# Kernel optimization log

Measured on AMD Instinct MI355X. Metric: run time of the kernel, lower is better.

## Reference

```python
import jax, jax.numpy as jnp
import numpy as np
from jax import lax

B_, N, C, NH, KB = 4096, 64, 192, 6, 8
WH = WW = 8  # win_size
HD = C // NH
KS = 5  # depthwise kernel size (distance=2)


def _rel_pos_index(wh, ww, k_bound):
    ch = np.arange(wh); cw = np.arange(ww)
    coords = np.stack(np.meshgrid(ch, cw, indexing='ij'))  # (2, wh, ww)
    cf = coords.reshape(2, -1)
    rel = cf[:, :, None] - cf[:, None, :]
    rel = np.clip(rel, -(k_bound - 1), k_bound - 1).transpose(1, 2, 0).astype(np.int32)
    rel[..., 0] += k_bound - 1
    rel[..., 1] += k_bound - 1
    rel[..., 0] *= 2 * k_bound - 1
    return rel.sum(-1)  # (N, N) indices into (2k-1)^2 table


def setup_inputs() -> dict:
    key = jax.random.key(0)
    ks = jax.random.split(key, 12)
    s = 0.02
    x = jax.random.normal(ks[0], (B_, N, C), dtype=jnp.float32)
    wq = jax.random.normal(ks[1], (C, C), dtype=jnp.float32) * s
    bq = jnp.zeros((C,), dtype=jnp.float32)
    wkv = jax.random.normal(ks[2], (C, 3 * C), dtype=jnp.float32) * s
    bkv = jnp.zeros((3 * C,), dtype=jnp.float32)
    rpb_table = jax.random.normal(ks[3], ((2 * KB - 1) * (2 * KB - 1), NH), dtype=jnp.float32) * s
    rel_index = jnp.asarray(_rel_pos_index(WH, WW, KB), dtype=jnp.int32)
    dw_w = jax.random.normal(ks[4], (C, 1, KS, KS), dtype=jnp.float32) * s   # depthwise, groups=C
    dw_b = jnp.zeros((C,), dtype=jnp.float32)
    pw_w = jax.random.normal(ks[5], (C, C // NH, 1, 1), dtype=jnp.float32) * s  # 1x1, groups=NH
    pw_b = jnp.zeros((C,), dtype=jnp.float32)
    proj_w = jax.random.normal(ks[6], (C, C), dtype=jnp.float32) * s
    proj_b = jnp.zeros((C,), dtype=jnp.float32)
    return dict(x=x, wq=wq, bq=bq, wkv=wkv, bkv=bkv, rpb_table=rpb_table,
                rel_index=rel_index, dw_w=dw_w, dw_b=dw_b, pw_w=pw_w, pw_b=pw_b,
                proj_w=proj_w, proj_b=proj_b)


def reference(x, wq, bq, wkv, bkv, rpb_table, rel_index, dw_w, dw_b, pw_w, pw_b, proj_w, proj_b):
    B, Nn, Cc = x.shape
    H = int(round(Nn ** 0.5))
    scale = (Cc // NH) ** -0.5
    # QKV projections
    q = (x @ wq + bq).reshape(B, Nn, NH, HD).transpose(0, 2, 1, 3)          # (B, nH, N, hd)
    kv = (x @ wkv + bkv).reshape(B, Nn, 3, NH, HD)
    k = kv[:, :, 0].transpose(0, 2, 1, 3)                                    # (B, nH, N, hd)
    v = kv[:, :, 1].transpose(0, 2, 1, 3)                                    # (B, nH, N, hd)
    v_r = kv[:, :, 2].transpose(0, 2, 3, 1).reshape(B, Cc, H, H)             # (B, C, H, H)
    # attention scores + relative position bias
    attn = jnp.einsum('bhnd,bhmd->bhnm', q * scale, k)
    bias = rpb_table[rel_index.reshape(-1)].reshape(Nn, Nn, NH).transpose(2, 0, 1)  # (nH, N, N)
    attn = jax.nn.softmax(attn + bias[None], axis=-1)
    # positional conv branch: depthwise 5x5 then grouped 1x1
    dn = ('NCHW', 'OIHW', 'NCHW')
    p = lax.conv_general_dilated(v_r, dw_w, (1, 1), 'SAME', dimension_numbers=dn,
                                 feature_group_count=Cc) + dw_b[None, :, None, None]
    p = lax.conv_general_dilated(p, pw_w, (1, 1), 'SAME', dimension_numbers=dn,
                                 feature_group_count=NH) + pw_b[None, :, None, None]
    position = p.reshape(B, Cc, Nn).transpose(0, 2, 1)                       # (B, N, C)
    out = jnp.einsum('bhnm,bhmd->bnhd', attn, v).reshape(B, Nn, Cc) + position
    return out @ proj_w + proj_b
```

## Files before the change

### kernel.cpp

```cpp
#include <hip/hip_runtime.h>

typedef _Float16 half8 __attribute__((ext_vector_type(8)));
typedef _Float16 half4 __attribute__((ext_vector_type(4)));
typedef _Float16 half2 __attribute__((ext_vector_type(2)));
typedef float floatx4 __attribute__((ext_vector_type(4)));

union H8 { half8 h8; half4 h4[2]; half2 h2[4]; int i[4]; };

__device__ __forceinline__ int packh2(float a, float b) {
    union { _Float16 h[2]; int i; } u;
    u.h[0] = (_Float16)a; u.h[1] = (_Float16)b;
    return u.i;
}

__device__ __forceinline__ half8 gather8(int idxA, int idxB, bool sel,
                                         int A0, int A1, int B0, int B1) {
    int a0 = __builtin_amdgcn_ds_bpermute(idxA, A0);
    int b0 = __builtin_amdgcn_ds_bpermute(idxA, B0);
    int a1 = __builtin_amdgcn_ds_bpermute(idxA, A1);
    int b1 = __builtin_amdgcn_ds_bpermute(idxA, B1);
    int a2 = __builtin_amdgcn_ds_bpermute(idxB, A0);
    int b2 = __builtin_amdgcn_ds_bpermute(idxB, B0);
    int a3 = __builtin_amdgcn_ds_bpermute(idxB, A1);
    int b3 = __builtin_amdgcn_ds_bpermute(idxB, B1);
    H8 u;
    u.i[0] = sel ? b0 : a0;
    u.i[1] = sel ? b1 : a1;
    u.i[2] = sel ? b2 : a2;
    u.i[3] = sel ? b3 : a3;
    return u.h8;
}


__global__ __launch_bounds__(512) void prep_kernel(
    const float* __restrict__ wq, const float* __restrict__ wkv,
    const float* __restrict__ proj_w, const float* __restrict__ rpb,
    const int* __restrict__ rel,
    const float* __restrict__ dw_w, const float* __restrict__ dw_b,
    const float* __restrict__ pw_w,
    _Float16* __restrict__ WtF, _Float16* __restrict__ PtF,
    float* __restrict__ biasF, _Float16* __restrict__ dwF,
    _Float16* __restrict__ dwbF, _Float16* __restrict__ pwF)
{
    int idx = blockIdx.x * 512 + threadIdx.x;
    if (idx < 147456) {
        int j = idx & 7, lane = (idx >> 3) & 63, t = idx >> 9;
        int ks = t % 6, nt = t / 6;
        int k = ks * 32 + (lane >> 4) * 8 + j;
        int n = nt * 16 + (lane & 15);
        float v = (n < 192) ? wq[k * 192 + n] : wkv[k * 576 + (n - 192)];
        WtF[idx] = (_Float16)v;
    } else if (idx < 184320) {
        int i2 = idx - 147456;
        int j = i2 & 7, lane = (i2 >> 3) & 63, t = i2 >> 9;
        int ks = t % 6, nt = t / 6;
        int k = ks * 32 + (lane >> 4) * 8 + j;
        int n = nt * 16 + (lane & 15);
        PtF[i2] = (_Float16)proj_w[k * 192 + n];
    } else if (idx < 208896) {
        int i2 = idx - 184320;
        int r = i2 & 3, lane = (i2 >> 2) & 63, t = i2 >> 8;
        int ntq = t & 3, mt = (t >> 2) & 3, h = t >> 4;
        int m = mt * 16 + (lane >> 4) * 4 + r;
        int n = ntq * 16 + (lane & 15);
        biasF[i2] = rpb[rel[n * 64 + m] * 6 + h];
    } else if (idx < 213696) {
        int i2 = idx - 208896;
        int j = i2 & 7, t = i2 >> 3;
        int tap = t % 25, gk = t / 25;
        int c = (gk >> 2) * 32 + (gk & 3) * 8 + j;
        dwF[i2] = (_Float16)dw_w[c * 25 + tap];
    } else if (idx < 213888) {
        int i2 = idx - 213696;
        int j = i2 & 7, gk = i2 >> 3;
        int c = (gk >> 2) * 32 + (gk & 3) * 8 + j;
        dwbF[i2] = (_Float16)dw_b[c];
    } else if (idx < 220032) {
        int i2 = idx - 213888;
        int j = i2 & 7, lane = (i2 >> 3) & 63, t = i2 >> 9;
        int ntc = t & 1, g = t >> 1;
        int oc = g * 32 + ntc * 16 + (lane & 15);
        int ic = (lane >> 4) * 8 + j;
        pwF[i2] = (_Float16)pw_w[oc * 32 + ic];
    }
}


#define XO   0
#define VRO  12800
#define SCR  25600
#define ZO   33280

__global__ __launch_bounds__(384, 3) void wa_main(
    const float* __restrict__ xg,
    const float* __restrict__ bq, const float* __restrict__ bkv,
    const float* __restrict__ proj_bg, const float* __restrict__ pw_b,
    const _Float16* __restrict__ WtF, const _Float16* __restrict__ PtF,
    const float* __restrict__ biasF,
    const _Float16* __restrict__ dwF, const _Float16* __restrict__ dwbF,
    const _Float16* __restrict__ pwF,
    float* __restrict__ outg)
{
    extern __shared__ unsigned char smem[];
    _Float16* sHalf = (_Float16*)smem;
    float* sBias = (float*)(smem + 66576);

    const int b    = blockIdx.x;
    const int tid  = threadIdx.x;
    const int lane = tid & 63;
    const int h    = tid >> 6;
    const int mrow = lane & 15;
    const int kq   = lane >> 4;
    const float scale = 0.17677669529663687f;
    _Float16* sS = sHalf + SCR + h * 1280;

    const float* xb = xg + (size_t)b * 12288;
    #pragma unroll
    for (int it = 0; it < 8; ++it) {
        int f4  = it * 384 + tid;
        int row = f4 / 48;
        int col = (f4 % 48) * 4;
        float4 v = ((const float4*)xb)[f4];
        half4 p;
        p[0] = (_Float16)v.x; p[1] = (_Float16)v.y;
        p[2] = (_Float16)v.z; p[3] = (_Float16)v.w;
        *(half4*)(sHalf + XO + row * 200 + col) = p;
    }
    for (int idx = tid; idx < 960; idx += 384) {
        float v;
        if      (idx < 192) v = bq[idx];
        else if (idx < 768) v = bkv[idx - 192];
        else                v = proj_bg[idx - 768];
        sBias[idx] = v;
    }
    if (tid < 8) sHalf[ZO + tid] = (_Float16)0.0f;
    __syncthreads();

    #pragma unroll
    for (int t = 0; t < 2; ++t) {
        int nt = 36 + 2 * h + t;
        half8 bf[6];
        #pragma unroll
        for (int ks = 0; ks < 6; ++ks)
            bf[ks] = ((const half8*)WtF)[(nt * 6 + ks) * 64 + lane];
        floatx4 binit = *(const floatx4*)(sBias + nt * 16 + kq * 4);
        #pragma unroll
        for (int mt4 = 0; mt4 < 4; ++mt4) {
            floatx4 acc = binit;
            #pragma unroll
            for (int ks = 0; ks < 6; ++ks) {
                half8 af = *(const half8*)(sHalf + XO + (mt4 * 16 + mrow) * 200 + ks * 32 + kq * 8);
                acc = __builtin_amdgcn_mfma_f32_16x16x32_f16(bf[ks], af, acc, 0, 0, 0);
            }
            union { int i2[2]; half4 h4; } u;
            u.i2[0] = packh2(acc[0], acc[1]);
            u.i2[1] = packh2(acc[2], acc[3]);
            *(half4*)(sHalf + VRO + (mt4 * 16 + mrow) * 200 + h * 32 + t * 16 + kq * 4) = u.h4;
        }
    }

    half8 aK[4], bQ[4];
    #pragma unroll
    for (int qk = 0; qk < 2; ++qk) {
        half8 bf2[2][6];
        #pragma unroll
        for (int t = 0; t < 2; ++t) {
            int nt = (qk == 0 ? 12 : 0) + 2 * h + t;
            #pragma unroll
            for (int ks = 0; ks < 6; ++ks)
                bf2[t][ks] = ((const half8*)WtF)[(nt * 6 + ks) * 64 + lane];
        }
        #pragma unroll
        for (int hf = 0; hf < 2; ++hf) {
            #pragma unroll
            for (int t = 0; t < 2; ++t) {
                int nt = (qk == 0 ? 12 : 0) + 2 * h + t;
                floatx4 binit = *(const floatx4*)(sBias + nt * 16 + kq * 4);
                #pragma unroll
                for (int mt2 = 0; mt2 < 2; ++mt2) {
                    int mt4 = hf * 2 + mt2;
                    floatx4 acc = binit;
                    #pragma unroll
                    for (int ks = 0; ks < 6; ++ks) {
                        half8 af = *(const half8*)(sHalf + XO + (mt4 * 16 + mrow) * 200 + ks * 32 + kq * 8);
                        acc = __builtin_amdgcn_mfma_f32_16x16x32_f16(bf2[t][ks], af, acc, 0, 0, 0);
                    }
                    if (qk == 1) {
                        acc[0] *= scale; acc[1] *= scale; acc[2] *= scale; acc[3] *= scale;
                    }
                    union { int i2[2]; half4 h4; } u;
                    u.i2[0] = packh2(acc[0], acc[1]);
                    u.i2[1] = packh2(acc[2], acc[3]);
                    *(half4*)(sS + (mt2 * 16 + mrow) * 40 + t * 16 + kq * 4) = u.h4;
                }
            }
            #pragma unroll
            for (int q2 = 0; q2 < 2; ++q2) {
                half8 f = *(const half8*)(sS + (q2 * 16 + mrow) * 40 + kq * 8);
                if (qk == 0) aK[hf * 2 + q2] = f;
                else         bQ[hf * 2 + q2] = f;
            }
        }
    }

    half8 bV[2][2];
    #pragma unroll
    for (int t = 0; t < 2; ++t) {
        int nt = 24 + 2 * h + t;
        half8 bf[6];
        #pragma unroll
        for (int ks = 0; ks < 6; ++ks)
            bf[ks] = ((const half8*)WtF)[(nt * 6 + ks) * 64 + lane];
        float bv = sBias[nt * 16 + mrow];
        #pragma unroll
        for (int mt = 0; mt < 4; ++mt) {
            floatx4 acc = {bv, bv, bv, bv};
            #pragma unroll
            for (int ks = 0; ks < 6; ++ks) {
                half8 af = *(const half8*)(sHalf + XO + (mt * 16 + mrow) * 200 + ks * 32 + kq * 8);
                acc = __builtin_amdgcn_mfma_f32_16x16x32_f16(af, bf[ks], acc, 0, 0, 0);
            }
            union { int i2[2]; half4 h4; } u;
            u.i2[0] = packh2(acc[0], acc[1]);
            u.i2[1] = packh2(acc[2], acc[3]);
            *(half4*)(sS + mrow * 72 + mt * 16 + kq * 4) = u.h4;
        }
        #pragma unroll
        for (int ks2 = 0; ks2 < 2; ++ks2)
            bV[t][ks2] = *(const half8*)(sS + mrow * 72 + ks2 * 32 + kq * 8);
    }

    const int cb32 = h * 32 + kq * 8;
    const half8* dwFp = (const half8*)dwF + (h * 4 + kq) * 25;
    H8 bini; bini.h8 = ((const half8*)dwbF)[h * 4 + kq];
    half2 cacc[4][4];
    #pragma unroll
    for (int mt = 0; mt < 4; ++mt)
        #pragma unroll
        for (int p = 0; p < 4; ++p) cacc[mt][p] = bini.h2[p];

    int ni[4], nj[4];
    #pragma unroll
    for (int mt = 0; mt < 4; ++mt) { int n = mt * 16 + mrow; ni[mt] = n >> 3; nj[mt] = n & 7; }

    #pragma unroll 5
    for (int t = 0; t < 25; ++t) {
        H8 w; w.h8 = dwFp[t];
        int di = t / 5 - 2, dj = t % 5 - 2;
        #pragma unroll
        for (int mt = 0; mt < 4; ++mt) {
            int ii = ni[mt] + di, jj = nj[mt] + dj;
            bool ok = ((unsigned)ii < 8u) & ((unsigned)jj < 8u);
            int off = ok ? (VRO + ((ii << 3) + jj) * 200 + cb32) : ZO;
            H8 d; d.h8 = *(const half8*)(sHalf + off);
            #pragma unroll
            for (int p = 0; p < 4; ++p) cacc[mt][p] += d.h2[p] * w.h2[p];
        }
    }
    half8 dwA[4];
    #pragma unroll
    for (int mt = 0; mt < 4; ++mt) {
        H8 u;
        #pragma unroll
        for (int p = 0; p < 4; ++p) u.h2[p] = cacc[mt][p];
        dwA[mt] = u.h8;
    }

    floatx4 accPV[4][2];
    #pragma unroll
    for (int ntc = 0; ntc < 2; ++ntc) {
        half8 pwB = ((const half8*)pwF)[(h * 2 + ntc) * 64 + lane];
        float4 pb4 = *(const float4*)(pw_b + h * 32 + ntc * 16 + kq * 4);
        #pragma unroll
        for (int mt = 0; mt < 4; ++mt) {
            floatx4 acc = {pb4.x, pb4.y, pb4.z, pb4.w};
            accPV[mt][ntc] = __builtin_amdgcn_mfma_f32_16x16x32_f16(pwB, dwA[mt], acc, 0, 0, 0);
        }
    }

    const int idxA = ((kq & 1) * 32 + mrow) * 4;
    const int idxB = idxA + 64;
    const bool sel = (kq >= 2);

    #pragma unroll
    for (int hf = 0; hf < 2; ++hf) {
        floatx4 stt[4][2];
        #pragma unroll
        for (int mtk = 0; mtk < 4; ++mtk)
            #pragma unroll
            for (int q2 = 0; q2 < 2; ++q2) {
                floatx4 bb = *(const floatx4*)(biasF + (((h * 4 + mtk) * 4 + hf * 2 + q2) * 64 + lane) * 4);
                stt[mtk][q2] = __builtin_amdgcn_mfma_f32_16x16x32_f16(aK[mtk], bQ[hf * 2 + q2], bb, 0, 0, 0);
            }

        #pragma unroll
        for (int q2 = 0; q2 < 2; ++q2) {
            float mx = stt[0][q2][0];
            #pragma unroll
            for (int mtk = 0; mtk < 4; ++mtk)
                #pragma unroll
                for (int r = 0; r < 4; ++r) mx = fmaxf(mx, stt[mtk][q2][r]);
            mx = fmaxf(mx, __shfl_xor(mx, 16));
            mx = fmaxf(mx, __shfl_xor(mx, 32));
            float sm = 0.0f;
            #pragma unroll
            for (int mtk = 0; mtk < 4; ++mtk)
                #pragma unroll
                for (int r = 0; r < 4; ++r) {
                    float e = __expf(stt[mtk][q2][r] - mx);
                    stt[mtk][q2][r] = e;
                    sm += e;
                }
            sm += __shfl_xor(sm, 16);
            sm += __shfl_xor(sm, 32);
            float inv = 1.0f / sm;
            #pragma unroll
            for (int mtk = 0; mtk < 4; ++mtk)
                #pragma unroll
                for (int r = 0; r < 4; ++r) stt[mtk][q2][r] *= inv;
        }

        int pk[4][2][2];
        #pragma unroll
        for (int mtk = 0; mtk < 4; ++mtk)
            #pragma unroll
            for (int q2 = 0; q2 < 2; ++q2) {
                pk[mtk][q2][0] = packh2(stt[mtk][q2][0], stt[mtk][q2][1]);
                pk[mtk][q2][1] = packh2(stt[mtk][q2][2], stt[mtk][q2][3]);
            }
        #pragma unroll
        for (int q2 = 0; q2 < 2; ++q2) {
            int mtq = hf * 2 + q2;
            #pragma unroll
            for (int ks2 = 0; ks2 < 2; ++ks2) {
                half8 aP = gather8(idxA, idxB, sel,
                                   pk[2 * ks2][q2][0],     pk[2 * ks2][q2][1],
                                   pk[2 * ks2 + 1][q2][0], pk[2 * ks2 + 1][q2][1]);
                #pragma unroll
                for (int ntd = 0; ntd < 2; ++ntd)
                    accPV[mtq][ntd] = __builtin_amdgcn_mfma_f32_16x16x32_f16(
                        bV[ntd][ks2], aP, accPV[mtq][ntd], 0, 0, 0);
            }
        }
    }

    #pragma unroll
    for (int mtq = 0; mtq < 4; ++mtq)
        #pragma unroll
        for (int ntd = 0; ntd < 2; ++ntd) {
            floatx4 o = accPV[mtq][ntd];
            union { int i2[2]; half4 h4; } u;
            u.i2[0] = packh2(o[0], o[1]);
            u.i2[1] = packh2(o[2], o[3]);
            *(half4*)(sHalf + VRO + (mtq * 16 + mrow) * 200 + h * 32 + ntd * 16 + kq * 4) = u.h4;
        }
    __syncthreads();

    float* og = outg + (size_t)b * 12288;
    #pragma unroll
    for (int tnt = 0; tnt < 2; ++tnt) {
        int nt = 2 * h + tnt;
        half8 bf[6];
        #pragma unroll
        for (int ks = 0; ks < 6; ++ks)
            bf[ks] = ((const half8*)PtF)[(nt * 6 + ks) * 64 + lane];
        float bv = sBias[768 + nt * 16 + mrow];
        #pragma unroll
        for (int mt = 0; mt < 4; ++mt) {
            floatx4 acc = {bv, bv, bv, bv};
            #pragma unroll
            for (int ks = 0; ks < 6; ++ks) {
                half8 af = *(const half8*)(sHalf + VRO + (mt * 16 + mrow) * 200 + ks * 32 + kq * 8);
                acc = __builtin_amdgcn_mfma_f32_16x16x32_f16(af, bf[ks], acc, 0, 0, 0);
            }
            int m0 = mt * 16 + kq * 4;
            #pragma unroll
            for (int r = 0; r < 4; ++r)
                og[(m0 + r) * 192 + nt * 16 + mrow] = acc[r];
        }
    }
}

extern "C" void kernel_launch(void* const* d_in, const int* in_sizes, int n_in,
                              void* d_out, int out_size, void* d_ws, size_t ws_size,
                              hipStream_t stream) {
    (void)in_sizes; (void)n_in; (void)out_size; (void)ws_size;
    const float* x      = (const float*)d_in[0];
    const float* wq     = (const float*)d_in[1];
    const float* bq     = (const float*)d_in[2];
    const float* wkv    = (const float*)d_in[3];
    const float* bkv    = (const float*)d_in[4];
    const float* rpb    = (const float*)d_in[5];
    const int*   rel    = (const int*)d_in[6];
    const float* dw_w   = (const float*)d_in[7];
    const float* dw_b   = (const float*)d_in[8];
    const float* pw_w   = (const float*)d_in[9];
    const float* pw_b   = (const float*)d_in[10];
    const float* proj_w = (const float*)d_in[11];
    const float* proj_b = (const float*)d_in[12];

    _Float16* WtF  = (_Float16*)d_ws;
    _Float16* PtF  = (_Float16*)((char*)d_ws + 294912);
    float*    biasF= (float*)((char*)d_ws + 368640);
    _Float16* dwF  = (_Float16*)((char*)d_ws + 466944);
    _Float16* dwbF = (_Float16*)((char*)d_ws + 476544);
    _Float16* pwF  = (_Float16*)((char*)d_ws + 476928);

    prep_kernel<<<430, 512, 0, stream>>>(wq, wkv, proj_w, rpb, rel, dw_w, dw_b, pw_w,
                                         WtF, PtF, biasF, dwF, dwbF, pwF);
    wa_main<<<4096, 384, 70416, stream>>>(x, bq, bkv, proj_b, pw_b,
                                          WtF, PtF, biasF, dwF, dwbF, pwF,
                                          (float*)d_out);
}
```

Baseline: 633.4 us.

## Cut register pressure: keep V fragments in LDS, load biases from global

Per-wave V fragments are no longer held in registers across the attention loop. They are stored in a larger per-wave LDS scratch and reloaded at each PV MFMA. Q/K weight fragments are now loaded per tile instead of two tiles at once, and the bias staging in shared memory is dropped in favor of direct global loads. The aim is to reduce VGPR pressure and spilling, at the cost of more LDS reads in the inner loop and a larger LDS allocation (about 80KB), which may limit blocks per CU.

New measurement: 627.0 us. Within noise of the previous version (-1.0%).

```diff
diff --git a/kernel.cpp b/kernel.cpp
--- a/kernel.cpp
+++ b/kernel.cpp
@@ -89,7 +89,7 @@
 #define XO   0
 #define VRO  12800
 #define SCR  25600
-#define ZO   33280
+#define ZO   40192
 
 __global__ __launch_bounds__(384, 3) void wa_main(
     const float* __restrict__ xg,
@@ -103,7 +103,6 @@
 {
     extern __shared__ unsigned char smem[];
     _Float16* sHalf = (_Float16*)smem;
-    float* sBias = (float*)(smem + 66576);
 
     const int b    = blockIdx.x;
     const int tid  = threadIdx.x;
@@ -112,7 +111,7 @@
     const int mrow = lane & 15;
     const int kq   = lane >> 4;
     const float scale = 0.17677669529663687f;
-    _Float16* sS = sHalf + SCR + h * 1280;
+    _Float16* sS = sHalf + SCR + h * 2432;
 
     const float* xb = xg + (size_t)b * 12288;
     #pragma unroll
@@ -126,13 +125,6 @@
         p[2] = (_Float16)v.z; p[3] = (_Float16)v.w;
         *(half4*)(sHalf + XO + row * 200 + col) = p;
     }
-    for (int idx = tid; idx < 960; idx += 384) {
-        float v;
-        if      (idx < 192) v = bq[idx];
-        else if (idx < 768) v = bkv[idx - 192];
-        else                v = proj_bg[idx - 768];
-        sBias[idx] = v;
-    }
     if (tid < 8) sHalf[ZO + tid] = (_Float16)0.0f;
     __syncthreads();
 
@@ -143,7 +135,8 @@
         #pragma unroll
         for (int ks = 0; ks < 6; ++ks)
             bf[ks] = ((const half8*)WtF)[(nt * 6 + ks) * 64 + lane];
-        floatx4 binit = *(const floatx4*)(sBias + nt * 16 + kq * 4);
+        float4 b4 = *(const float4*)(bkv + nt * 16 - 192 + kq * 4);
+        floatx4 binit = {b4.x, b4.y, b4.z, b4.w};
         #pragma unroll
         for (int mt4 = 0; mt4 < 4; ++mt4) {
             floatx4 acc = binit;
@@ -162,20 +155,18 @@
     half8 aK[4], bQ[4];
     #pragma unroll
     for (int qk = 0; qk < 2; ++qk) {
-        half8 bf2[2][6];
-        #pragma unroll
-        for (int t = 0; t < 2; ++t) {
-            int nt = (qk == 0 ? 12 : 0) + 2 * h + t;
-            #pragma unroll
-            for (int ks = 0; ks < 6; ++ks)
-                bf2[t][ks] = ((const half8*)WtF)[(nt * 6 + ks) * 64 + lane];
-        }
         #pragma unroll
         for (int hf = 0; hf < 2; ++hf) {
             #pragma unroll
             for (int t = 0; t < 2; ++t) {
                 int nt = (qk == 0 ? 12 : 0) + 2 * h + t;
-                floatx4 binit = *(const floatx4*)(sBias + nt * 16 + kq * 4);
+                half8 bf[6];
+                #pragma unroll
+                for (int ks = 0; ks < 6; ++ks)
+                    bf[ks] = ((const half8*)WtF)[(nt * 6 + ks) * 64 + lane];
+                const float* bptr = (qk == 0) ? (bkv + nt * 16 - 192) : (bq + nt * 16);
+                float4 b4 = *(const float4*)(bptr + kq * 4);
+                floatx4 binit = {b4.x, b4.y, b4.z, b4.w};
                 #pragma unroll
                 for (int mt2 = 0; mt2 < 2; ++mt2) {
                     int mt4 = hf * 2 + mt2;
@@ -183,7 +174,7 @@
                     #pragma unroll
                     for (int ks = 0; ks < 6; ++ks) {
                         half8 af = *(const half8*)(sHalf + XO + (mt4 * 16 + mrow) * 200 + ks * 32 + kq * 8);
-                        acc = __builtin_amdgcn_mfma_f32_16x16x32_f16(bf2[t][ks], af, acc, 0, 0, 0);
+                        acc = __builtin_amdgcn_mfma_f32_16x16x32_f16(bf[ks], af, acc, 0, 0, 0);
                     }
                     if (qk == 1) {
                         acc[0] *= scale; acc[1] *= scale; acc[2] *= scale; acc[3] *= scale;
@@ -203,7 +194,6 @@
         }
     }
 
-    half8 bV[2][2];
     #pragma unroll
     for (int t = 0; t < 2; ++t) {
         int nt = 24 + 2 * h + t;
@@ -211,7 +201,7 @@
         #pragma unroll
         for (int ks = 0; ks < 6; ++ks)
             bf[ks] = ((const half8*)WtF)[(nt * 6 + ks) * 64 + lane];
-        float bv = sBias[nt * 16 + mrow];
+        float bv = bkv[nt * 16 - 192 + mrow];
         #pragma unroll
         for (int mt = 0; mt < 4; ++mt) {
             floatx4 acc = {bv, bv, bv, bv};
@@ -223,11 +213,8 @@
             union { int i2[2]; half4 h4; } u;
             u.i2[0] = packh2(acc[0], acc[1]);
             u.i2[1] = packh2(acc[2], acc[3]);
-            *(half4*)(sS + mrow * 72 + mt * 16 + kq * 4) = u.h4;
-        }
-        #pragma unroll
-        for (int ks2 = 0; ks2 < 2; ++ks2)
-            bV[t][ks2] = *(const half8*)(sS + mrow * 72 + ks2 * 32 + kq * 8);
+            *(half4*)(sS + mrow * 152 + t * 72 + mt * 16 + kq * 4) = u.h4;
+        }
     }
 
     const int cb32 = h * 32 + kq * 8;
@@ -337,9 +324,11 @@
                                    pk[2 * ks2][q2][0],     pk[2 * ks2][q2][1],
                                    pk[2 * ks2 + 1][q2][0], pk[2 * ks2 + 1][q2][1]);
                 #pragma unroll
-                for (int ntd = 0; ntd < 2; ++ntd)
+                for (int ntd = 0; ntd < 2; ++ntd) {
+                    half8 bVv = *(const half8*)(sS + mrow * 152 + ntd * 72 + ks2 * 32 + kq * 8);
                     accPV[mtq][ntd] = __builtin_amdgcn_mfma_f32_16x16x32_f16(
-                        bV[ntd][ks2], aP, accPV[mtq][ntd], 0, 0, 0);
+                        bVv, aP, accPV[mtq][ntd], 0, 0, 0);
+                }
             }
         }
     }
@@ -364,7 +353,7 @@
         #pragma unroll
         for (int ks = 0; ks < 6; ++ks)
             bf[ks] = ((const half8*)PtF)[(nt * 6 + ks) * 64 + lane];
-        float bv = sBias[768 + nt * 16 + mrow];
+        float bv = proj_bg[nt * 16 + mrow];
         #pragma unroll
         for (int mt = 0; mt < 4; ++mt) {
             floatx4 acc = {bv, bv, bv, bv};
@@ -408,7 +397,7 @@
 
     prep_kernel<<<430, 512, 0, stream>>>(wq, wkv, proj_w, rpb, rel, dw_w, dw_b, pw_w,
                                          WtF, PtF, biasF, dwF, dwbF, pwF);
-    wa_main<<<4096, 384, 70416, stream>>>(x, bq, bkv, proj_b, pw_b,
+    wa_main<<<4096, 384, 80400, stream>>>(x, bq, bkv, proj_b, pw_b,
                                           WtF, PtF, biasF, dwF, dwbF, pwF,
                                           (float*)d_out);
 }
```
